# Kernel optimization log

Hardware: AMD Instinct MI355X
Metric: run time of the kernel (lower is better)

Reference implementation:

```python
import jax, jax.numpy as jnp
import numpy as np

N_NODES = 50000
N_EDGES = 800000

def _graph_conv(x, W, b, src, dst, n_nodes):
    # DGL GraphConv, norm='both': D_dst^{-1/2} * A * D_src^{-1/2} * X * W + b
    ones_e = jnp.ones((src.shape[0],), dtype=x.dtype)
    deg_out = jax.ops.segment_sum(ones_e, src, num_segments=n_nodes)
    deg_in = jax.ops.segment_sum(ones_e, dst, num_segments=n_nodes)
    norm_src = jnp.maximum(deg_out, 1.0) ** -0.5  # [N]
    norm_dst = jnp.maximum(deg_in, 1.0) ** -0.5   # [N]
    xs = x * norm_src[:, None]                    # pre-normalize
    agg = jax.ops.segment_sum(xs[src], dst, num_segments=n_nodes)  # SpMM
    agg = agg * norm_dst[:, None]
    return agg @ W + b

def setup_inputs() -> dict:
    key = jax.random.key(0)
    k1, k2, k3, k4, k5 = jax.random.split(key, 5)
    features = jax.random.normal(k1, (N_NODES, 128), dtype=jnp.float32)
    W1 = jax.random.normal(k2, (128, 256), dtype=jnp.float32) * (1.0 / np.sqrt(128))
    b1 = jnp.zeros((256,), dtype=jnp.float32)
    W2 = jax.random.normal(k3, (256, 40), dtype=jnp.float32) * (1.0 / np.sqrt(256))
    b2 = jnp.zeros((40,), dtype=jnp.float32)
    src = jax.random.randint(k4, (N_EDGES,), 0, N_NODES, dtype=jnp.int32)
    dst = jax.random.randint(k5, (N_EDGES,), 0, N_NODES, dtype=jnp.int32)
    return {"features": features, "W1": W1, "b1": b1, "W2": W2, "b2": b2,
            "src": src, "dst": dst}

def reference(features, W1, b1, W2, b2, src, dst):
    n = features.shape[0]
    # layer 1: GraphConv with activation=relu, then an extra F.relu (idempotent)
    h = _graph_conv(features, W1, b1, src, dst, n)
    h = jax.nn.relu(h)
    # dropout(p=0.5): identity in eval mode (deterministic reference)
    h = _graph_conv(h, W2, b2, src, dst, n)
    return jax.nn.log_softmax(h, axis=1)
```

## Files before the change

### kernel.cpp

```cpp
#include <hip/hip_runtime.h>
#include <cstdint>
#include <cstddef>

#define N_NODES 50000
#define N_EDGES 800000
#define F_IN    128
#define F_HID   256
#define F_OUT   40
#define NB      196
#define NCOPY   8
#define SREP    50176

__global__ __launch_bounds__(256) void degree_kernel(
    const int* __restrict__ src, const int* __restrict__ dst,
    int* __restrict__ degc_out, int* __restrict__ degc_in) {
  int b = blockIdx.x;
  int i = b * 256 + threadIdx.x;
  int k = b & (NCOPY - 1);
  if (i < N_EDGES) {
    atomicAdd(&degc_out[k * SREP + src[i]], 1);
    atomicAdd(&degc_in[k * SREP + dst[i]], 1);
  }
}

__global__ __launch_bounds__(256) void reduce_kernel(
    const int* __restrict__ degc_out, const int* __restrict__ degc_in,
    int* __restrict__ deg_in_tot, float* __restrict__ norm_src,
    float* __restrict__ norm_dst) {
  int v = blockIdx.x * 256 + threadIdx.x;
  if (v >= N_NODES) return;
  int di = 0, dq = 0;
#pragma unroll
  for (int k = 0; k < NCOPY; ++k) {
    di += degc_in[k * SREP + v];
    dq += degc_out[k * SREP + v];
  }
  deg_in_tot[v] = di;
  norm_dst[v] = 1.0f / sqrtf(fmaxf((float)di, 1.0f));
  norm_src[v] = 1.0f / sqrtf(fmaxf((float)dq, 1.0f));
}

__global__ __launch_bounds__(256) void block_sum_kernel(
    const int* __restrict__ deg_in, int* __restrict__ bsum) {
  __shared__ int arr[256];
  int node = blockIdx.x * 256 + threadIdx.x;
  arr[threadIdx.x] = (node < N_NODES) ? deg_in[node] : 0;
  __syncthreads();
  for (int off = 128; off > 0; off >>= 1) {
    if (threadIdx.x < off) arr[threadIdx.x] += arr[threadIdx.x + off];
    __syncthreads();
  }
  if (threadIdx.x == 0) bsum[blockIdx.x] = arr[0];
}

__global__ __launch_bounds__(256) void scan_bsum_kernel(int* __restrict__ bsum) {
  __shared__ int arr[256];
  int tid = threadIdx.x;
  int v = (tid < NB) ? bsum[tid] : 0;
  arr[tid] = v;
  __syncthreads();
  for (int off = 1; off < 256; off <<= 1) {
    int t = (tid >= off) ? arr[tid - off] : 0;
    __syncthreads();
    arr[tid] += t;
    __syncthreads();
  }
  if (tid < NB) bsum[tid] = arr[tid] - v;
}

__global__ __launch_bounds__(256) void finalize_kernel(
    const int* __restrict__ deg_in_tot, const int* __restrict__ degc_in,
    const int* __restrict__ bsum, int* __restrict__ row_ptr,
    int* __restrict__ cur) {
  __shared__ int arr[256];
  int tid = threadIdx.x;
  int node = blockIdx.x * 256 + tid;
  int di = (node < N_NODES) ? deg_in_tot[node] : 0;
  arr[tid] = di;
  __syncthreads();
  for (int off = 1; off < 256; off <<= 1) {
    int t = (tid >= off) ? arr[tid - off] : 0;
    __syncthreads();
    arr[tid] += t;
    __syncthreads();
  }
  if (node < N_NODES) {
    int rp = bsum[blockIdx.x] + arr[tid] - di;
    row_ptr[node] = rp;
    int b = rp;
#pragma unroll
    for (int k = 0; k < NCOPY; ++k) {
      cur[k * SREP + node] = b;
      b += degc_in[k * SREP + node];
    }
  }
  if (blockIdx.x == 0 && tid == 0) row_ptr[N_NODES] = N_EDGES;
}

__global__ __launch_bounds__(256) void scatter_kernel(
    const int* __restrict__ src, const int* __restrict__ dst,
    int* __restrict__ cur, int* __restrict__ csr_src) {
  int b = blockIdx.x;
  int i = b * 256 + threadIdx.x;
  int k = b & (NCOPY - 1);
  if (i < N_EDGES) {
    int d = dst[i];
    int p = atomicAdd(&cur[k * SREP + d], 1);
    csr_src[p] = src[i];
  }
}

__global__ __launch_bounds__(256) void prescale_kernel(
    const float* __restrict__ feat, const float* __restrict__ norm_src,
    float* __restrict__ xs) {
  int i = blockIdx.x * 256 + threadIdx.x;
  int row = i >> 5;
  float4 v = ((const float4*)feat)[i];
  float ns = norm_src[row];
  v.x *= ns; v.y *= ns; v.z *= ns; v.w *= ns;
  ((float4*)xs)[i] = v;
}

__global__ __launch_bounds__(256) void agg1_kernel(
    const float* __restrict__ xs, const int* __restrict__ row_ptr,
    const int* __restrict__ csr_src, const float* __restrict__ norm_dst,
    float* __restrict__ out) {
  int wid = (blockIdx.x * 256 + threadIdx.x) >> 6;
  if (wid >= N_NODES) return;
  int lane = threadIdx.x & 63;
  int g = lane >> 5;
  int l32 = lane & 31;
  int beg = row_ptr[wid], end = row_ptr[wid + 1];
  float4 acc = make_float4(0.f, 0.f, 0.f, 0.f);
  int e = beg + g;
  if (e < end) {
    int s = csr_src[e];
    while (true) {
      int en = e + 2;
      int sn = (en < end) ? csr_src[en] : 0;
      float4 f = *(const float4*)(xs + (size_t)s * F_IN + (l32 << 2));
      acc.x += f.x; acc.y += f.y; acc.z += f.z; acc.w += f.w;
      if (en >= end) break;
      e = en; s = sn;
    }
  }
  acc.x += __shfl_xor(acc.x, 32);
  acc.y += __shfl_xor(acc.y, 32);
  acc.z += __shfl_xor(acc.z, 32);
  acc.w += __shfl_xor(acc.w, 32);
  if (g == 0) {
    float nd = norm_dst[wid];
    acc.x *= nd; acc.y *= nd; acc.z *= nd; acc.w *= nd;
    *(float4*)(out + (size_t)wid * F_IN + (l32 << 2)) = acc;
  }
}

__global__ __launch_bounds__(256) void gemm1_kernel(
    const float* __restrict__ A, const float* __restrict__ B,
    const float* __restrict__ bias, float* __restrict__ C, int M) {
  constexpr int BM = 128, BN = 64, BK = 32, TM = 8, TN = 4;
  constexpr int N = F_HID, K = F_IN;
  __shared__ float As[BK][BM + 4];
  __shared__ float Bs[BK][BN];
  int tid = threadIdx.x;
  int tx = tid % (BN / TN);
  int ty = tid / (BN / TN);
  int row0 = blockIdx.x * BM;
  int col0 = blockIdx.y * BN;
  float acc[TM][TN];
#pragma unroll
  for (int i = 0; i < TM; ++i)
#pragma unroll
    for (int j = 0; j < TN; ++j) acc[i][j] = 0.f;

  for (int k0 = 0; k0 < K; k0 += BK) {
#pragma unroll
    for (int idx = tid; idx < BM * BK / 4; idx += 256) {
      int r = idx / (BK / 4);
      int c4 = idx % (BK / 4);
      int row = row0 + r;
      float4 v = (row < M) ? *(const float4*)(A + (size_t)row * K + k0 + c4 * 4)
                           : make_float4(0.f, 0.f, 0.f, 0.f);
      As[c4 * 4 + 0][r] = v.x;
      As[c4 * 4 + 1][r] = v.y;
      As[c4 * 4 + 2][r] = v.z;
      As[c4 * 4 + 3][r] = v.w;
    }
#pragma unroll
    for (int idx = tid; idx < BK * BN / 4; idx += 256) {
      int r = idx / (BN / 4);
      int c4 = idx % (BN / 4);
      *(float4*)(&Bs[r][c4 * 4]) =
          *(const float4*)(B + (size_t)(k0 + r) * N + col0 + c4 * 4);
    }
    __syncthreads();
#pragma unroll
    for (int k = 0; k < BK; ++k) {
      float4 a0 = *(const float4*)(&As[k][ty * TM]);
      float4 a1 = *(const float4*)(&As[k][ty * TM + 4]);
      float4 b0 = *(const float4*)(&Bs[k][tx * TN]);
      float a[TM] = {a0.x, a0.y, a0.z, a0.w, a1.x, a1.y, a1.z, a1.w};
      float b[TN] = {b0.x, b0.y, b0.z, b0.w};
#pragma unroll
      for (int i = 0; i < TM; ++i)
#pragma unroll
        for (int j = 0; j < TN; ++j) acc[i][j] += a[i] * b[j];
    }
    __syncthreads();
  }

#pragma unroll
  for (int i = 0; i < TM; ++i) {
    int row = row0 + ty * TM + i;
    if (row >= M) continue;
    float4 bv = *(const float4*)(bias + col0 + tx * TN);
    float4 v = make_float4(fmaxf(acc[i][0] + bv.x, 0.f),
                           fmaxf(acc[i][1] + bv.y, 0.f),
                           fmaxf(acc[i][2] + bv.z, 0.f),
                           fmaxf(acc[i][3] + bv.w, 0.f));
    *(float4*)(C + (size_t)row * N + col0 + tx * TN) = v;
  }
}

__global__ __launch_bounds__(320) void gemm2_kernel(
    const float* __restrict__ A, const float* __restrict__ B,
    const float* __restrict__ rowscale, float* __restrict__ C, int M) {
  constexpr int BM = 128, BN = 40, BK = 32, TM = 4, TN = 4;
  constexpr int N = F_OUT, K = F_HID;
  __shared__ float As[BK][BM + 4];
  __shared__ float Bs[BK][BN];
  int tid = threadIdx.x;
  int tx = tid % (BN / TN);
  int ty = tid / (BN / TN);
  int row0 = blockIdx.x * BM;
  float acc[TM][TN];
#pragma unroll
  for (int i = 0; i < TM; ++i)
#pragma unroll
    for (int j = 0; j < TN; ++j) acc[i][j] = 0.f;

  for (int k0 = 0; k0 < K; k0 += BK) {
    for (int idx = tid; idx < BM * BK / 4; idx += 320) {
      int r = idx / (BK / 4);
      int c4 = idx % (BK / 4);
      int row = row0 + r;
      float4 v = (row < M) ? *(const float4*)(A + (size_t)row * K + k0 + c4 * 4)
                           : make_float4(0.f, 0.f, 0.f, 0.f);
      As[c4 * 4 + 0][r] = v.x;
      As[c4 * 4 + 1][r] = v.y;
      As[c4 * 4 + 2][r] = v.z;
      As[c4 * 4 + 3][r] = v.w;
    }
    {
      int r = tid / 10;
      int c4 = tid % 10;
      *(float4*)(&Bs[r][c4 * 4]) =
          *(const float4*)(B + (size_t)(k0 + r) * N + c4 * 4);
    }
    __syncthreads();
#pragma unroll
    for (int k = 0; k < BK; ++k) {
      float4 a0 = *(const float4*)(&As[k][ty * TM]);
      float4 b0 = *(const float4*)(&Bs[k][tx * TN]);
      float a[TM] = {a0.x, a0.y, a0.z, a0.w};
      float b[TN] = {b0.x, b0.y, b0.z, b0.w};
#pragma unroll
      for (int i = 0; i < TM; ++i)
#pragma unroll
        for (int j = 0; j < TN; ++j) acc[i][j] += a[i] * b[j];
    }
    __syncthreads();
  }

#pragma unroll
  for (int i = 0; i < TM; ++i) {
    int row = row0 + ty * TM + i;
    if (row >= M) continue;
    float rs = rowscale[row];
    float4 v = make_float4(acc[i][0] * rs, acc[i][1] * rs,
                           acc[i][2] * rs, acc[i][3] * rs);
    *(float4*)(C + (size_t)row * N + tx * TN) = v;
  }
}

__global__ __launch_bounds__(256) void agg2_softmax_kernel(
    const float* __restrict__ t, const int* __restrict__ row_ptr,
    const int* __restrict__ csr_src, const float* __restrict__ norm_dst,
    const float* __restrict__ b2, float* __restrict__ out) {
  int wid = (blockIdx.x * 256 + threadIdx.x) >> 6;
  if (wid >= N_NODES) return;
  int lane = threadIdx.x & 63;
  int g = lane >> 4;
  int l16 = lane & 15;
  bool act = l16 < 10;
  int beg = row_ptr[wid], end = row_ptr[wid + 1];
  float4 acc = make_float4(0.f, 0.f, 0.f, 0.f);
  for (int e = beg + g; e < end; e += 4) {
    int s = csr_src[e];
    if (act) {
      float4 f = *(const float4*)(t + (size_t)s * F_OUT + (l16 << 2));
      acc.x += f.x; acc.y += f.y; acc.z += f.z; acc.w += f.w;
    }
  }
#pragma unroll
  for (int off = 16; off <= 32; off <<= 1) {
    acc.x += __shfl_xor(acc.x, off);
    acc.y += __shfl_xor(acc.y, off);
    acc.z += __shfl_xor(acc.z, off);
    acc.w += __shfl_xor(acc.w, off);
  }
  float nd = norm_dst[wid];
  float4 v;
  if (act) {
    float4 bv = *(const float4*)(b2 + (l16 << 2));
    v = make_float4(acc.x * nd + bv.x, acc.y * nd + bv.y,
                    acc.z * nd + bv.z, acc.w * nd + bv.w);
  } else {
    v = make_float4(-INFINITY, -INFINITY, -INFINITY, -INFINITY);
  }
  float m = fmaxf(fmaxf(v.x, v.y), fmaxf(v.z, v.w));
#pragma unroll
  for (int off = 1; off <= 8; off <<= 1) m = fmaxf(m, __shfl_xor(m, off));
  float ex = act ? (expf(v.x - m) + expf(v.y - m) + expf(v.z - m) + expf(v.w - m)) : 0.f;
#pragma unroll
  for (int off = 1; off <= 8; off <<= 1) ex += __shfl_xor(ex, off);
  float ls = logf(ex);
  if (g == 0 && act) {
    float4 r = make_float4(v.x - m - ls, v.y - m - ls, v.z - m - ls, v.w - m - ls);
    *(float4*)(out + (size_t)wid * F_OUT + (l16 << 2)) = r;
  }
}

extern "C" void kernel_launch(void* const* d_in, const int* in_sizes, int n_in,
                              void* d_out, int out_size, void* d_ws, size_t ws_size,
                              hipStream_t stream) {
  const float* feat = (const float*)d_in[0];
  const float* W1   = (const float*)d_in[1];
  const float* b1   = (const float*)d_in[2];
  const float* W2   = (const float*)d_in[3];
  const float* b2   = (const float*)d_in[4];
  const int*   src  = (const int*)d_in[5];
  const int*   dst  = (const int*)d_in[6];
  float* out = (float*)d_out;

  char* p = (char*)d_ws;
  auto alloc = [&](size_t bytes) {
    char* r = p;
    p += (bytes + 255) & ~(size_t)255;
    return r;
  };
  int*   degc_out = (int*)alloc((size_t)NCOPY * SREP * 4);
  int*   degc_in  = (int*)alloc((size_t)NCOPY * SREP * 4);
  int*   cur      = (int*)alloc((size_t)NCOPY * SREP * 4);
  int*   deg_in_tot = (int*)alloc((size_t)N_NODES * 4);
  int*   bsum     = (int*)alloc((size_t)NB * 4);
  int*   row_ptr  = (int*)alloc((size_t)(N_NODES + 1) * 4);
  int*   csr_src  = (int*)alloc((size_t)N_EDGES * 4);
  float* norm_src = (float*)alloc((size_t)N_NODES * 4);
  float* norm_dst = (float*)alloc((size_t)N_NODES * 4);
  float* t        = (float*)alloc((size_t)N_NODES * F_OUT * 4);
  float* xs       = (float*)alloc((size_t)N_NODES * F_HID * 4);
  float* h        = xs;
  float* agg1     = (float*)alloc((size_t)N_NODES * F_IN * 4);

  size_t zero_bytes = (size_t)((char*)cur - (char*)degc_out);
  hipMemsetAsync(degc_out, 0, zero_bytes, stream);

  degree_kernel<<<(N_EDGES + 255) / 256, 256, 0, stream>>>(src, dst, degc_out, degc_in);
  reduce_kernel<<<NB, 256, 0, stream>>>(degc_out, degc_in, deg_in_tot, norm_src, norm_dst);
  block_sum_kernel<<<NB, 256, 0, stream>>>(deg_in_tot, bsum);
  scan_bsum_kernel<<<1, 256, 0, stream>>>(bsum);
  finalize_kernel<<<NB, 256, 0, stream>>>(deg_in_tot, degc_in, bsum, row_ptr, cur);
  scatter_kernel<<<(N_EDGES + 255) / 256, 256, 0, stream>>>(src, dst, cur, csr_src);
  prescale_kernel<<<N_NODES * (F_IN / 4) / 256, 256, 0, stream>>>(feat, norm_src, xs);
  agg1_kernel<<<(N_NODES * 64) / 256 + 1, 256, 0, stream>>>(xs, row_ptr, csr_src,
                                                            norm_dst, agg1);
  gemm1_kernel<<<dim3((N_NODES + 127) / 128, F_HID / 64), 256, 0, stream>>>(
      agg1, W1, b1, h, N_NODES);
  gemm2_kernel<<<(N_NODES + 127) / 128, 320, 0, stream>>>(h, W2, norm_src, t, N_NODES);
  agg2_softmax_kernel<<<(N_NODES * 64) / 256 + 1, 256, 0, stream>>>(
      t, row_ptr, csr_src, norm_dst, b2, out);
}
```

Before: 383.1 us.

## Enlarge GEMM register tiles and dual-accumulate edge gathers in aggregation kernels

```diff
diff --git a/kernel.cpp b/kernel.cpp
--- a/kernel.cpp
+++ b/kernel.cpp
@@ -131,53 +131,58 @@
   int g = lane >> 5;
   int l32 = lane & 31;
   int beg = row_ptr[wid], end = row_ptr[wid + 1];
-  float4 acc = make_float4(0.f, 0.f, 0.f, 0.f);
+  float4 accA = make_float4(0.f, 0.f, 0.f, 0.f);
+  float4 accB = make_float4(0.f, 0.f, 0.f, 0.f);
   int e = beg + g;
+  for (; e + 2 < end; e += 4) {
+    int s0 = csr_src[e];
+    int s1 = csr_src[e + 2];
+    float4 f0 = *(const float4*)(xs + (size_t)s0 * F_IN + (l32 << 2));
+    float4 f1 = *(const float4*)(xs + (size_t)s1 * F_IN + (l32 << 2));
+    accA.x += f0.x; accA.y += f0.y; accA.z += f0.z; accA.w += f0.w;
+    accB.x += f1.x; accB.y += f1.y; accB.z += f1.z; accB.w += f1.w;
+  }
   if (e < end) {
-    int s = csr_src[e];
-    while (true) {
-      int en = e + 2;
-      int sn = (en < end) ? csr_src[en] : 0;
-      float4 f = *(const float4*)(xs + (size_t)s * F_IN + (l32 << 2));
-      acc.x += f.x; acc.y += f.y; acc.z += f.z; acc.w += f.w;
-      if (en >= end) break;
-      e = en; s = sn;
-    }
-  }
-  acc.x += __shfl_xor(acc.x, 32);
-  acc.y += __shfl_xor(acc.y, 32);
-  acc.z += __shfl_xor(acc.z, 32);
-  acc.w += __shfl_xor(acc.w, 32);
+    int s0 = csr_src[e];
+    float4 f0 = *(const float4*)(xs + (size_t)s0 * F_IN + (l32 << 2));
+    accA.x += f0.x; accA.y += f0.y; accA.z += f0.z; accA.w += f0.w;
+  }
+  accA.x += accB.x; accA.y += accB.y; accA.z += accB.z; accA.w += accB.w;
+  accA.x += __shfl_xor(accA.x, 32);
+  accA.y += __shfl_xor(accA.y, 32);
+  accA.z += __shfl_xor(accA.z, 32);
+  accA.w += __shfl_xor(accA.w, 32);
   if (g == 0) {
     float nd = norm_dst[wid];
-    acc.x *= nd; acc.y *= nd; acc.z *= nd; acc.w *= nd;
-    *(float4*)(out + (size_t)wid * F_IN + (l32 << 2)) = acc;
+    accA.x *= nd; accA.y *= nd; accA.z *= nd; accA.w *= nd;
+    *(float4*)(out + (size_t)wid * F_IN + (l32 << 2)) = accA;
   }
 }
 
 __global__ __launch_bounds__(256) void gemm1_kernel(
     const float* __restrict__ A, const float* __restrict__ B,
     const float* __restrict__ bias, float* __restrict__ C, int M) {
-  constexpr int BM = 128, BN = 64, BK = 32, TM = 8, TN = 4;
+  constexpr int BM = 128, BN = 128, BK = 32;
   constexpr int N = F_HID, K = F_IN;
   __shared__ float As[BK][BM + 4];
   __shared__ float Bs[BK][BN];
   int tid = threadIdx.x;
-  int tx = tid % (BN / TN);
-  int ty = tid / (BN / TN);
+  int tx = tid & 15;
+  int ty = tid >> 4;
   int row0 = blockIdx.x * BM;
   int col0 = blockIdx.y * BN;
-  float acc[TM][TN];
-#pragma unroll
-  for (int i = 0; i < TM; ++i)
-#pragma unroll
-    for (int j = 0; j < TN; ++j) acc[i][j] = 0.f;
+  float acc[8][8];
+#pragma unroll
+  for (int i = 0; i < 8; ++i)
+#pragma unroll
+    for (int j = 0; j < 8; ++j) acc[i][j] = 0.f;
 
   for (int k0 = 0; k0 < K; k0 += BK) {
 #pragma unroll
-    for (int idx = tid; idx < BM * BK / 4; idx += 256) {
-      int r = idx / (BK / 4);
-      int c4 = idx % (BK / 4);
+    for (int it = 0; it < 4; ++it) {
+      int idx = tid + it * 256;
+      int r = idx >> 3;
+      int c4 = idx & 7;
       int row = row0 + r;
       float4 v = (row < M) ? *(const float4*)(A + (size_t)row * K + k0 + c4 * 4)
                            : make_float4(0.f, 0.f, 0.f, 0.f);
@@ -187,62 +192,67 @@
       As[c4 * 4 + 3][r] = v.w;
     }
 #pragma unroll
-    for (int idx = tid; idx < BK * BN / 4; idx += 256) {
-      int r = idx / (BN / 4);
-      int c4 = idx % (BN / 4);
+    for (int it = 0; it < 4; ++it) {
+      int idx = tid + it * 256;
+      int r = idx >> 5;
+      int c4 = idx & 31;
       *(float4*)(&Bs[r][c4 * 4]) =
           *(const float4*)(B + (size_t)(k0 + r) * N + col0 + c4 * 4);
     }
     __syncthreads();
-#pragma unroll
+#pragma unroll 8
     for (int k = 0; k < BK; ++k) {
-      float4 a0 = *(const float4*)(&As[k][ty * TM]);
-      float4 a1 = *(const float4*)(&As[k][ty * TM + 4]);
-      float4 b0 = *(const float4*)(&Bs[k][tx * TN]);
-      float a[TM] = {a0.x, a0.y, a0.z, a0.w, a1.x, a1.y, a1.z, a1.w};
-      float b[TN] = {b0.x, b0.y, b0.z, b0.w};
-#pragma unroll
-      for (int i = 0; i < TM; ++i)
-#pragma unroll
-        for (int j = 0; j < TN; ++j) acc[i][j] += a[i] * b[j];
-    }
-    __syncthreads();
-  }
-
-#pragma unroll
-  for (int i = 0; i < TM; ++i) {
-    int row = row0 + ty * TM + i;
+      float4 a0 = *(const float4*)(&As[k][ty * 8]);
+      float4 a1 = *(const float4*)(&As[k][ty * 8 + 4]);
+      float a[8] = {a0.x, a0.y, a0.z, a0.w, a1.x, a1.y, a1.z, a1.w};
+      float b[8];
+#pragma unroll
+      for (int j = 0; j < 8; ++j) b[j] = Bs[k][tx + 16 * j];
+#pragma unroll
+      for (int i = 0; i < 8; ++i)
+#pragma unroll
+        for (int j = 0; j < 8; ++j) acc[i][j] += a[i] * b[j];
+    }
+    __syncthreads();
+  }
+
+  float bv[8];
+#pragma unroll
+  for (int j = 0; j < 8; ++j) bv[j] = bias[col0 + tx + 16 * j];
+#pragma unroll
+  for (int i = 0; i < 8; ++i) {
+    int row = row0 + ty * 8 + i;
     if (row >= M) continue;
-    float4 bv = *(const float4*)(bias + col0 + tx * TN);
-    float4 v = make_float4(fmaxf(acc[i][0] + bv.x, 0.f),
-                           fmaxf(acc[i][1] + bv.y, 0.f),
-                           fmaxf(acc[i][2] + bv.z, 0.f),
-                           fmaxf(acc[i][3] + bv.w, 0.f));
-    *(float4*)(C + (size_t)row * N + col0 + tx * TN) = v;
-  }
-}
-
-__global__ __launch_bounds__(320) void gemm2_kernel(
+#pragma unroll
+    for (int j = 0; j < 8; ++j) {
+      C[(size_t)row * N + col0 + tx + 16 * j] = fmaxf(acc[i][j] + bv[j], 0.f);
+    }
+  }
+}
+
+__global__ __launch_bounds__(128) void gemm2_kernel(
     const float* __restrict__ A, const float* __restrict__ B,
     const float* __restrict__ rowscale, float* __restrict__ C, int M) {
-  constexpr int BM = 128, BN = 40, BK = 32, TM = 4, TN = 4;
+  constexpr int BM = 128, BK = 32;
   constexpr int N = F_OUT, K = F_HID;
   __shared__ float As[BK][BM + 4];
-  __shared__ float Bs[BK][BN];
+  __shared__ float Bs[BK][N];
   int tid = threadIdx.x;
-  int tx = tid % (BN / TN);
-  int ty = tid / (BN / TN);
+  int tx = tid & 7;
+  int ty = tid >> 3;
   int row0 = blockIdx.x * BM;
-  float acc[TM][TN];
-#pragma unroll
-  for (int i = 0; i < TM; ++i)
-#pragma unroll
-    for (int j = 0; j < TN; ++j) acc[i][j] = 0.f;
+  float acc[8][5];
+#pragma unroll
+  for (int i = 0; i < 8; ++i)
+#pragma unroll
+    for (int j = 0; j < 5; ++j) acc[i][j] = 0.f;
 
   for (int k0 = 0; k0 < K; k0 += BK) {
-    for (int idx = tid; idx < BM * BK / 4; idx += 320) {
-      int r = idx / (BK / 4);
-      int c4 = idx % (BK / 4);
+#pragma unroll
+    for (int it = 0; it < 8; ++it) {
+      int idx = tid + it * 128;
+      int r = idx >> 3;
+      int c4 = idx & 7;
       int row = row0 + r;
       float4 v = (row < M) ? *(const float4*)(A + (size_t)row * K + k0 + c4 * 4)
                            : make_float4(0.f, 0.f, 0.f, 0.f);
@@ -251,35 +261,42 @@
       As[c4 * 4 + 2][r] = v.z;
       As[c4 * 4 + 3][r] = v.w;
     }
-    {
-      int r = tid / 10;
-      int c4 = tid % 10;
-      *(float4*)(&Bs[r][c4 * 4]) =
-          *(const float4*)(B + (size_t)(k0 + r) * N + c4 * 4);
-    }
-    __syncthreads();
-#pragma unroll
+#pragma unroll
+    for (int it = 0; it < 3; ++it) {
+      int idx = tid + it * 128;
+      if (idx < 320) {
+        int r = idx / 10;
+        int c4 = idx % 10;
+        *(float4*)(&Bs[r][c4 * 4]) =
+            *(const float4*)(B + (size_t)(k0 + r) * N + c4 * 4);
+      }
+    }
+    __syncthreads();
+#pragma unroll 8
     for (int k = 0; k < BK; ++k) {
-      float4 a0 = *(const float4*)(&As[k][ty * TM]);
-      float4 b0 = *(const float4*)(&Bs[k][tx * TN]);
-      float a[TM] = {a0.x, a0.y, a0.z, a0.w};
-      float b[TN] = {b0.x, b0.y, b0.z, b0.w};
-#pragma unroll
-      for (int i = 0; i < TM; ++i)
-#pragma unroll
-        for (int j = 0; j < TN; ++j) acc[i][j] += a[i] * b[j];
-    }
-    __syncthreads();
-  }
-
-#pragma unroll
-  for (int i = 0; i < TM; ++i) {
-    int row = row0 + ty * TM + i;
+      float4 a0 = *(const float4*)(&As[k][ty * 8]);
+      float4 a1 = *(const float4*)(&As[k][ty * 8 + 4]);
+      float a[8] = {a0.x, a0.y, a0.z, a0.w, a1.x, a1.y, a1.z, a1.w};
+      float b[5];
+#pragma unroll
+      for (int j = 0; j < 5; ++j) b[j] = Bs[k][tx + 8 * j];
+#pragma unroll
+      for (int i = 0; i < 8; ++i)
+#pragma unroll
+        for (int j = 0; j < 5; ++j) acc[i][j] += a[i] * b[j];
+    }
+    __syncthreads();
+  }
+
+#pragma unroll
+  for (int i = 0; i < 8; ++i) {
+    int row = row0 + ty * 8 + i;
     if (row >= M) continue;
     float rs = rowscale[row];
-    float4 v = make_float4(acc[i][0] * rs, acc[i][1] * rs,
-                           acc[i][2] * rs, acc[i][3] * rs);
-    *(float4*)(C + (size_t)row * N + tx * TN) = v;
+#pragma unroll
+    for (int j = 0; j < 5; ++j) {
+      C[(size_t)row * N + tx + 8 * j] = acc[i][j] * rs;
+    }
   }
 }
 
@@ -294,27 +311,40 @@
   int l16 = lane & 15;
   bool act = l16 < 10;
   int beg = row_ptr[wid], end = row_ptr[wid + 1];
-  float4 acc = make_float4(0.f, 0.f, 0.f, 0.f);
-  for (int e = beg + g; e < end; e += 4) {
-    int s = csr_src[e];
+  float4 accA = make_float4(0.f, 0.f, 0.f, 0.f);
+  float4 accB = make_float4(0.f, 0.f, 0.f, 0.f);
+  int e = beg + g;
+  for (; e + 4 < end; e += 8) {
+    int s0 = csr_src[e];
+    int s1 = csr_src[e + 4];
     if (act) {
-      float4 f = *(const float4*)(t + (size_t)s * F_OUT + (l16 << 2));
-      acc.x += f.x; acc.y += f.y; acc.z += f.z; acc.w += f.w;
-    }
-  }
+      float4 f0 = *(const float4*)(t + (size_t)s0 * F_OUT + (l16 << 2));
+      float4 f1 = *(const float4*)(t + (size_t)s1 * F_OUT + (l16 << 2));
+      accA.x += f0.x; accA.y += f0.y; accA.z += f0.z; accA.w += f0.w;
+      accB.x += f1.x; accB.y += f1.y; accB.z += f1.z; accB.w += f1.w;
+    }
+  }
+  if (e < end) {
+    int s0 = csr_src[e];
+    if (act) {
+      float4 f0 = *(const float4*)(t + (size_t)s0 * F_OUT + (l16 << 2));
+      accA.x += f0.x; accA.y += f0.y; accA.z += f0.z; accA.w += f0.w;
+    }
+  }
+  accA.x += accB.x; accA.y += accB.y; accA.z += accB.z; accA.w += accB.w;
 #pragma unroll
   for (int off = 16; off <= 32; off <<= 1) {
-    acc.x += __shfl_xor(acc.x, off);
-    acc.y += __shfl_xor(acc.y, off);
-    acc.z += __shfl_xor(acc.z, off);
-    acc.w += __shfl_xor(acc.w, off);
+    accA.x += __shfl_xor(accA.x, off);
+    accA.y += __shfl_xor(accA.y, off);
+    accA.z += __shfl_xor(accA.z, off);
+    accA.w += __shfl_xor(accA.w, off);
   }
   float nd = norm_dst[wid];
   float4 v;
   if (act) {
     float4 bv = *(const float4*)(b2 + (l16 << 2));
-    v = make_float4(acc.x * nd + bv.x, acc.y * nd + bv.y,
-                    acc.z * nd + bv.z, acc.w * nd + bv.w);
+    v = make_float4(accA.x * nd + bv.x, accA.y * nd + bv.y,
+                    accA.z * nd + bv.z, accA.w * nd + bv.w);
   } else {
     v = make_float4(-INFINITY, -INFINITY, -INFINITY, -INFINITY);
   }
@@ -375,9 +405,9 @@
   prescale_kernel<<<N_NODES * (F_IN / 4) / 256, 256, 0, stream>>>(feat, norm_src, xs);
   agg1_kernel<<<(N_NODES * 64) / 256 + 1, 256, 0, stream>>>(xs, row_ptr, csr_src,
                                                             norm_dst, agg1);
-  gemm1_kernel<<<dim3((N_NODES + 127) / 128, F_HID / 64), 256, 0, stream>>>(
+  gemm1_kernel<<<dim3((N_NODES + 127) / 128, F_HID / 128), 256, 0, stream>>>(
       agg1, W1, b1, h, N_NODES);
-  gemm2_kernel<<<(N_NODES + 127) / 128, 320, 0, stream>>>(h, W2, norm_src, t, N_NODES);
+  gemm2_kernel<<<(N_NODES + 127) / 128, 128, 0, stream>>>(h, W2, norm_src, t, N_NODES);
   agg2_softmax_kernel<<<(N_NODES * 64) / 256 + 1, 256, 0, stream>>>(
       t, row_ptr, csr_src, norm_dst, b2, out);
 }
```

Result: slower. 405.7 us (+5.9%).
